# Performance work log

Measured on AMD Instinct MI355X. Metric: run time of the kernel, lower is better.

The kernel has to match this reference:

```python
import jax, jax.numpy as jnp
import numpy as np

N = 50000

def _add_self_loops(edge_index, n):
    loop = jnp.arange(n, dtype=edge_index.dtype)
    src = jnp.concatenate([edge_index[0], loop])
    dst = jnp.concatenate([edge_index[1], loop])
    return src, dst

def _gcn_layer(x, src, dst, norm, W, b, n):
    h = x @ W                                  # [N, out]
    msg = h[src] * norm[:, None]               # [E+N, out] gather + scale
    out = jax.ops.segment_sum(msg, dst, num_segments=n)  # scatter-add
    return out + b

def _gcn_norm(src, dst, n):
    # symmetric normalization D^-1/2 (A+I) D^-1/2 (PyG GCNConv default)
    deg = jax.ops.segment_sum(jnp.ones_like(dst, dtype=jnp.float32), dst, num_segments=n)
    dinv = jnp.where(deg > 0, jax.lax.rsqrt(jnp.maximum(deg, 1.0)), 0.0)
    return dinv[src] * dinv[dst]

def setup_inputs() -> dict:
    key = jax.random.key(0)
    ks = jax.random.split(key, 4)
    x = jax.random.normal(ks[0], (N, 64), dtype=jnp.float32)
    edge_index = jax.random.randint(ks[1], (2, 800000), 0, N, dtype=jnp.int64)
    W1 = jax.random.normal(ks[2], (64, 128), dtype=jnp.float32) * (1.0 / np.sqrt(64))
    b1 = jnp.zeros((128,), dtype=jnp.float32)
    W2 = jax.random.normal(ks[3], (128, 64), dtype=jnp.float32) * (1.0 / np.sqrt(128))
    b2 = jnp.zeros((64,), dtype=jnp.float32)
    return {"x": x, "edge_index": edge_index, "W1": W1, "b1": b1, "W2": W2, "b2": b2}

def reference(x, edge_index, W1, b1, W2, b2):
    n = x.shape[0]
    src, dst = _add_self_loops(edge_index, n)
    norm = _gcn_norm(src, dst, n)
    h = _gcn_layer(x, src, dst, norm, W1, b1, n)
    h = jax.nn.relu(h)
    # dropout with p=0 (eval) is identity
    h = _gcn_layer(h, src, dst, norm, W2, b2, n)
    return jax.nn.relu(h)
```

## Files before the change

### kernel.cpp

```cpp
#include <hip/hip_runtime.h>
#include <hip/hip_fp16.h>
#include <cstddef>
#include <cstdint>

static inline int divup(int a, int b) { return (a + b - 1) / b; }

#define CAP 64
#define EPB 4096
#define BSH 8

typedef _Float16 h2v __attribute__((ext_vector_type(2)));

__device__ inline float fdot2f(unsigned int a, unsigned int b, float c) {
#if __has_builtin(__builtin_amdgcn_fdot2)
    return __builtin_amdgcn_fdot2(__builtin_bit_cast(h2v, a),
                                  __builtin_bit_cast(h2v, b), c, false);
#else
    __half2 ha = __builtin_bit_cast(__half2, a);
    __half2 hb = __builtin_bit_cast(__half2, b);
    float2 fa = __half22float2(ha), fb = __half22float2(hb);
    return fmaf(fa.y, fb.y, fmaf(fa.x, fb.x, c));
#endif
}

__global__ __launch_bounds__(256) void k_bin(const int* __restrict__ src,
                                             const int* __restrict__ dst,
                                             int2* __restrict__ staging,
                                             int* __restrict__ runoff,
                                             int* __restrict__ runlen,
                                             int E, int nbuck, int NB) {
    __shared__ int hist[256];
    __shared__ int scan[256];
    const int t = threadIdx.x;
    const int blk = blockIdx.x;
    const int e0 = blk * EPB;

    int2 ed[16];
    int cb[16];
    #pragma unroll
    for (int j = 0; j < 16; ++j) {
        int idx = e0 + j * 256 + t;
        if (idx < E) {
            ed[j].x = src[idx];
            ed[j].y = dst[idx];
            cb[j] = ed[j].y >> BSH;
        } else {
            cb[j] = -1;
        }
    }
    hist[t] = 0;
    __syncthreads();
    #pragma unroll
    for (int j = 0; j < 16; ++j)
        if (cb[j] >= 0) atomicAdd(&hist[cb[j]], 1);
    __syncthreads();
    scan[t] = hist[t];
    __syncthreads();
    for (int d = 1; d < 256; d <<= 1) {
        int v = (t >= d) ? scan[t - d] : 0;
        __syncthreads();
        scan[t] += v;
        __syncthreads();
    }
    int base = scan[t] - hist[t];
    if (t < nbuck) {
        runoff[t * NB + blk] = base;
        runlen[t * NB + blk] = hist[t];
    }
    hist[t] = base;
    __syncthreads();
    #pragma unroll
    for (int j = 0; j < 16; ++j) {
        if (cb[j] >= 0) {
            int p = atomicAdd(&hist[cb[j]], 1);
            staging[e0 + p] = ed[j];
        }
    }
}

__global__ __launch_bounds__(256) void k_build(const int2* __restrict__ staging,
                                               const int* __restrict__ runoff,
                                               const int* __restrict__ runlen,
                                               const float* __restrict__ x,
                                               int* __restrict__ eidx,
                                               int* __restrict__ cnt,
                                               float* __restrict__ dinv,
                                               __half* __restrict__ xh,
                                               int n, int NB) {
    __shared__ int runstart[512 + 1];
    __shared__ int runbase[512];
    __shared__ int cnt_l[256];
    __shared__ float sdinv[256];
    const int t = threadIdx.x;
    const int b = blockIdx.x;
    const int node0 = b << BSH;

    for (int r = t; r < NB; r += 256) {
        runbase[r] = runoff[b * NB + r];
        runstart[r] = runlen[b * NB + r];
    }
    cnt_l[t] = 0;
    __syncthreads();
    if (t == 0) {
        int run = 0;
        for (int r = 0; r < NB; ++r) { int l = runstart[r]; runstart[r] = run; run += l; }
        runstart[NB] = run;
    }
    __syncthreads();
    const int L = runstart[NB];
    for (int i = t; i < L; i += 256) {
        int lo = 0, hi = NB - 1;
        while (lo < hi) { int mid = (lo + hi + 1) >> 1; if (runstart[mid] <= i) lo = mid; else hi = mid - 1; }
        int2 ed = staging[lo * EPB + runbase[lo] + (i - runstart[lo])];
        int p = atomicAdd(&cnt_l[ed.y - node0], 1);
        if (p < CAP) eidx[(size_t)ed.y * CAP + p] = ed.x;
    }
    __syncthreads();
    int node = node0 + t;
    float di_t = rsqrtf((float)(cnt_l[t] + 1));
    sdinv[t] = di_t;
    if (node < n) {
        cnt[node] = cnt_l[t];
        dinv[node] = di_t;
    }
    __syncthreads();
    for (int i = t; i < 256 * 16; i += 256) {
        int lr = i >> 4, c4 = (i & 15) * 4;
        int nd = node0 + lr;
        if (nd < n) {
            float4 v = *reinterpret_cast<const float4*>(x + (size_t)nd * 64 + c4);
            float di = sdinv[lr];
            __half2 h0 = __floats2half2_rn(v.x * di, v.y * di);
            __half2 h1 = __floats2half2_rn(v.z * di, v.w * di);
            *reinterpret_cast<__half2*>(xh + (size_t)nd * 64 + c4)     = h0;
            *reinterpret_cast<__half2*>(xh + (size_t)nd * 64 + c4 + 2) = h1;
        }
    }
}

__device__ inline void acc8(uint4 u, float a[8]) {
    float2 f0 = __half22float2(*reinterpret_cast<const __half2*>(&u.x));
    float2 f1 = __half22float2(*reinterpret_cast<const __half2*>(&u.y));
    float2 f2 = __half22float2(*reinterpret_cast<const __half2*>(&u.z));
    float2 f3 = __half22float2(*reinterpret_cast<const __half2*>(&u.w));
    a[0] += f0.x; a[1] += f0.y; a[2] += f1.x; a[3] += f1.y;
    a[4] += f2.x; a[5] += f2.y; a[6] += f3.x; a[7] += f3.y;
}

template <bool FINAL>
__global__ __launch_bounds__(256) void k_aggh(const int* __restrict__ cnt,
                                              const int* __restrict__ eidx,
                                              const __half* __restrict__ in16,
                                              const float* __restrict__ dinv,
                                              const float* __restrict__ bias,
                                              void* __restrict__ outp, int n) {
    int t = blockIdx.x * blockDim.x + threadIdx.x;
    int node = t >> 3;
    if (node >= n) return;
    int lane = t & 7;
    const int hoff = lane * 8;
    float a[8] = {0.f, 0.f, 0.f, 0.f, 0.f, 0.f, 0.f, 0.f};
    acc8(*reinterpret_cast<const uint4*>(in16 + (size_t)node * 64 + hoff), a);
    const int b = node * CAP;
    const int eN = b + min(cnt[node], CAP);
    int e = b;
    for (; e + 4 <= eN; e += 4) {
        int s0 = __builtin_nontemporal_load(eidx + e);
        int s1 = __builtin_nontemporal_load(eidx + e + 1);
        int s2 = __builtin_nontemporal_load(eidx + e + 2);
        int s3 = __builtin_nontemporal_load(eidx + e + 3);
        uint4 u0 = *reinterpret_cast<const uint4*>(in16 + (size_t)s0 * 64 + hoff);
        uint4 u1 = *reinterpret_cast<const uint4*>(in16 + (size_t)s1 * 64 + hoff);
        uint4 u2 = *reinterpret_cast<const uint4*>(in16 + (size_t)s2 * 64 + hoff);
        uint4 u3 = *reinterpret_cast<const uint4*>(in16 + (size_t)s3 * 64 + hoff);
        acc8(u0, a); acc8(u1, a); acc8(u2, a); acc8(u3, a);
    }
    for (; e < eN; ++e) {
        int s = __builtin_nontemporal_load(eidx + e);
        acc8(*reinterpret_cast<const uint4*>(in16 + (size_t)s * 64 + hoff), a);
    }
    float di = dinv[node];
    if (FINAL) {
        float* out64 = (float*)outp;
        float4 r0, r1;
        const float4 b0 = *reinterpret_cast<const float4*>(bias + hoff);
        const float4 b1 = *reinterpret_cast<const float4*>(bias + hoff + 4);
        r0.x = fmaxf(fmaf(a[0], di, b0.x), 0.f); r0.y = fmaxf(fmaf(a[1], di, b0.y), 0.f);
        r0.z = fmaxf(fmaf(a[2], di, b0.z), 0.f); r0.w = fmaxf(fmaf(a[3], di, b0.w), 0.f);
        r1.x = fmaxf(fmaf(a[4], di, b1.x), 0.f); r1.y = fmaxf(fmaf(a[5], di, b1.y), 0.f);
        r1.z = fmaxf(fmaf(a[6], di, b1.z), 0.f); r1.w = fmaxf(fmaf(a[7], di, b1.w), 0.f);
        *reinterpret_cast<float4*>(out64 + (size_t)node * 64 + hoff)     = r0;
        *reinterpret_cast<float4*>(out64 + (size_t)node * 64 + hoff + 4) = r1;
    } else {
        unsigned int* out16 = (unsigned int*)outp;
        __half2 p0 = __floats2half2_rn(a[0] * di, a[1] * di);
        __half2 p1 = __floats2half2_rn(a[2] * di, a[3] * di);
        __half2 p2 = __floats2half2_rn(a[4] * di, a[5] * di);
        __half2 p3 = __floats2half2_rn(a[6] * di, a[7] * di);
        uint4 o;
        o.x = __builtin_bit_cast(unsigned int, p0);
        o.y = __builtin_bit_cast(unsigned int, p1);
        o.z = __builtin_bit_cast(unsigned int, p2);
        o.w = __builtin_bit_cast(unsigned int, p3);
        *reinterpret_cast<uint4*>(out16 + (size_t)node * 32 + lane * 4) = o;
    }
}

__global__ void k_wconv(const float* __restrict__ W1, const float* __restrict__ W2,
                        unsigned int* __restrict__ w1p, unsigned int* __restrict__ w2p) {
    int i = blockIdx.x * blockDim.x + threadIdx.x;
    if (i < 32 * 128) {
        int kp = i >> 7, c = i & 127;
        __half2 h = __floats2half2_rn(W1[(size_t)(2 * kp) * 128 + c], W1[(size_t)(2 * kp + 1) * 128 + c]);
        w1p[i] = __builtin_bit_cast(unsigned int, h);
    } else if (i < 32 * 128 + 64 * 64) {
        int j = i - 32 * 128;
        int kp = j >> 6, c = j & 63;
        __half2 h = __floats2half2_rn(W2[(size_t)(2 * kp) * 64 + c], W2[(size_t)(2 * kp + 1) * 64 + c]);
        w2p[j] = __builtin_bit_cast(unsigned int, h);
    }
}

__global__ __launch_bounds__(256) void k_mlp(const __half* __restrict__ axh,
                                             const unsigned int* __restrict__ w1p,
                                             const unsigned int* __restrict__ w2p,
                                             const float* __restrict__ b1,
                                             const float* __restrict__ dinv,
                                             __half* __restrict__ hs2h, int n) {
    __shared__ unsigned int sW1[32 * 128];
    __shared__ unsigned int sW2[64 * 64];
    __shared__ unsigned int sA[32 * 68];
    __shared__ unsigned int sH[64 * 68];
    const int t = threadIdx.x;
    const int r0 = blockIdx.x * 64;
    {
        uint4* d1 = reinterpret_cast<uint4*>(sW1);
        const uint4* s1 = reinterpret_cast<const uint4*>(w1p);
        for (int i = t; i < 1024; i += 256) d1[i] = s1[i];
        uint4* d2 = reinterpret_cast<uint4*>(sW2);
        const uint4* s2 = reinterpret_cast<const uint4*>(w2p);
        for (int i = t; i < 1024; i += 256) d2[i] = s2[i];
    }
    const unsigned int* axu = reinterpret_cast<const unsigned int*>(axh);
    for (int i = t; i < 2048; i += 256) {
        int row = i >> 5, kp = i & 31;
        int gr = r0 + row;
        sA[kp * 68 + row] = (gr < n) ? axu[(size_t)gr * 32 + kp] : 0u;
    }
    __syncthreads();
    const int tx = t & 15, ty = t >> 4;
    float acc[4][8] = {};
    #pragma unroll 8
    for (int kp = 0; kp < 32; ++kp) {
        uint4 a4 = *reinterpret_cast<const uint4*>(&sA[kp * 68 + ty * 4]);
        uint4 wA = *reinterpret_cast<const uint4*>(&sW1[kp * 128 + tx * 4]);
        uint4 wB = *reinterpret_cast<const uint4*>(&sW1[kp * 128 + 64 + tx * 4]);
        unsigned int av[4] = {a4.x, a4.y, a4.z, a4.w};
        unsigned int wv[8] = {wA.x, wA.y, wA.z, wA.w, wB.x, wB.y, wB.z, wB.w};
        #pragma unroll
        for (int r = 0; r < 4; ++r)
            #pragma unroll
            for (int c = 0; c < 8; ++c)
                acc[r][c] = fdot2f(av[r], wv[c], acc[r][c]);
    }
    const float4 bb0 = *reinterpret_cast<const float4*>(b1 + tx * 4);
    const float4 bb1 = *reinterpret_cast<const float4*>(b1 + 64 + tx * 4);
    #pragma unroll
    for (int r = 0; r < 4; ++r) {
        int row = ty * 4 + r;
        float h0 = fmaxf(acc[r][0] + bb0.x, 0.f), h1 = fmaxf(acc[r][1] + bb0.y, 0.f);
        float h2 = fmaxf(acc[r][2] + bb0.z, 0.f), h3 = fmaxf(acc[r][3] + bb0.w, 0.f);
        float h4 = fmaxf(acc[r][4] + bb1.x, 0.f), h5 = fmaxf(acc[r][5] + bb1.y, 0.f);
        float h6 = fmaxf(acc[r][6] + bb1.z, 0.f), h7 = fmaxf(acc[r][7] + bb1.w, 0.f);
        __half2 p;
        p = __floats2half2_rn(h0, h1); sH[(2 * tx + 0) * 68 + row]  = __builtin_bit_cast(unsigned int, p);
        p = __floats2half2_rn(h2, h3); sH[(2 * tx + 1) * 68 + row]  = __builtin_bit_cast(unsigned int, p);
        p = __floats2half2_rn(h4, h5); sH[(32 + 2 * tx) * 68 + row] = __builtin_bit_cast(unsigned int, p);
        p = __floats2half2_rn(h6, h7); sH[(33 + 2 * tx) * 68 + row] = __builtin_bit_cast(unsigned int, p);
    }
    __syncthreads();
    float acc2[4][4] = {};
    #pragma unroll 8
    for (int kp = 0; kp < 64; ++kp) {
        uint4 a4 = *reinterpret_cast<const uint4*>(&sH[kp * 68 + ty * 4]);
        uint4 w4 = *reinterpret_cast<const uint4*>(&sW2[kp * 64 + tx * 4]);
        unsigned int av[4] = {a4.x, a4.y, a4.z, a4.w};
        unsigned int wv[4] = {w4.x, w4.y, w4.z, w4.w};
        #pragma unroll
        for (int r = 0; r < 4; ++r)
            #pragma unroll
            for (int c = 0; c < 4; ++c)
                acc2[r][c] = fdot2f(av[r], wv[c], acc2[r][c]);
    }
    #pragma unroll
    for (int r = 0; r < 4; ++r) {
        int row = r0 + ty * 4 + r;
        if (row < n) {
            float di = dinv[row];
            __half2 q0 = __floats2half2_rn(acc2[r][0] * di, acc2[r][1] * di);
            __half2 q1 = __floats2half2_rn(acc2[r][2] * di, acc2[r][3] * di);
            uint2 o;
            o.x = __builtin_bit_cast(unsigned int, q0);
            o.y = __builtin_bit_cast(unsigned int, q1);
            *reinterpret_cast<uint2*>(hs2h + (size_t)row * 64 + tx * 4) = o;
        }
    }
}

extern "C" void kernel_launch(void* const* d_in, const int* in_sizes, int n_in,
                              void* d_out, int out_size, void* d_ws, size_t ws_size,
                              hipStream_t stream) {
    const float* x  = (const float*)d_in[0];
    const int*   ei = (const int*)d_in[1];
    const float* W1 = (const float*)d_in[2];
    const float* b1 = (const float*)d_in[3];
    const float* W2 = (const float*)d_in[4];
    const float* b2 = (const float*)d_in[5];
    float* out = (float*)d_out;

    const int n = in_sizes[0] / 64;
    const int E = in_sizes[1] / 2;
    const int* src = ei;
    const int* dst = ei + E;

    const int NB = divup(E, EPB);
    const int nbuck = divup(n, 1 << BSH);

    char* ws = (char*)d_ws;
    size_t off = 0;
    auto alloc = [&](size_t bytes) { void* p = ws + off; off = (off + bytes + 255) & ~(size_t)255; return p; };
    int*    cnt     = (int*)   alloc((size_t)n * 4);
    float*  dinv    = (float*) alloc((size_t)n * 4);
    int2*   staging = (int2*)  alloc((size_t)NB * EPB * 8);
    int*    runoff  = (int*)   alloc((size_t)nbuck * NB * 4);
    int*    runlen  = (int*)   alloc((size_t)nbuck * NB * 4);
    int*    eidx    = (int*)   alloc((size_t)n * CAP * 4);
    __half* xh      = (__half*)alloc((size_t)n * 64 * 2);
    __half* axh     = (__half*)alloc((size_t)n * 64 * 2);
    unsigned int* w1p = (unsigned int*)alloc(32 * 128 * 4);
    unsigned int* w2p = (unsigned int*)alloc(64 * 64 * 4);
    __half* hs2h    = xh;

    k_bin  <<<NB, 256, 0, stream>>>(src, dst, staging, runoff, runlen, E, nbuck, NB);
    k_build<<<nbuck, 256, 0, stream>>>(staging, runoff, runlen, x, eidx, cnt, dinv, xh, n, NB);
    k_wconv<<<32, 256, 0, stream>>>(W1, W2, w1p, w2p);

    k_aggh<false><<<divup(n * 8, 256), 256, 0, stream>>>(cnt, eidx, xh, dinv, nullptr, axh, n);

    k_mlp<<<divup(n, 64), 256, 0, stream>>>(axh, w1p, w2p, b1, dinv, hs2h, n);

    k_aggh<true><<<divup(n * 8, 256), 256, 0, stream>>>(cnt, eidx, hs2h, dinv, b2, out, n);
}
```

Before: 117.2 us.

## Fuse first aggregation into MLP, fold weight conversion into binning, parallel scan

```diff
diff --git a/kernel.cpp b/kernel.cpp
--- a/kernel.cpp
+++ b/kernel.cpp
@@ -28,11 +28,32 @@
                                              int2* __restrict__ staging,
                                              int* __restrict__ runoff,
                                              int* __restrict__ runlen,
+                                             const float* __restrict__ W1,
+                                             const float* __restrict__ W2,
+                                             unsigned int* __restrict__ w1p,
+                                             unsigned int* __restrict__ w2p,
                                              int E, int nbuck, int NB) {
+    const int t = threadIdx.x;
+    const int blk = blockIdx.x;
+    if (blk == NB) {
+        for (int i = t; i < 32 * 128 + 64 * 64; i += 256) {
+            if (i < 32 * 128) {
+                int kp = i >> 7, c = i & 127;
+                __half2 h = __floats2half2_rn(W1[(size_t)(2 * kp) * 128 + c],
+                                              W1[(size_t)(2 * kp + 1) * 128 + c]);
+                w1p[i] = __builtin_bit_cast(unsigned int, h);
+            } else {
+                int j = i - 32 * 128;
+                int kp = j >> 6, c = j & 63;
+                __half2 h = __floats2half2_rn(W2[(size_t)(2 * kp) * 64 + c],
+                                              W2[(size_t)(2 * kp + 1) * 64 + c]);
+                w2p[j] = __builtin_bit_cast(unsigned int, h);
+            }
+        }
+        return;
+    }
     __shared__ int hist[256];
     __shared__ int scan[256];
-    const int t = threadIdx.x;
-    const int blk = blockIdx.x;
     const int e0 = blk * EPB;
 
     int2 ed[16];
@@ -89,23 +110,26 @@
                                                int n, int NB) {
     __shared__ int runstart[512 + 1];
     __shared__ int runbase[512];
+    __shared__ int sscan[256];
     __shared__ int cnt_l[256];
     __shared__ float sdinv[256];
     const int t = threadIdx.x;
     const int b = blockIdx.x;
     const int node0 = b << BSH;
 
-    for (int r = t; r < NB; r += 256) {
-        runbase[r] = runoff[b * NB + r];
-        runstart[r] = runlen[b * NB + r];
-    }
+    for (int r = t; r < NB; r += 256) runbase[r] = runoff[b * NB + r];
+    int myv = (t < NB) ? runlen[b * NB + t] : 0;
+    sscan[t] = myv;
     cnt_l[t] = 0;
     __syncthreads();
-    if (t == 0) {
-        int run = 0;
-        for (int r = 0; r < NB; ++r) { int l = runstart[r]; runstart[r] = run; run += l; }
-        runstart[NB] = run;
-    }
+    for (int d = 1; d < 256; d <<= 1) {
+        int u = (t >= d) ? sscan[t - d] : 0;
+        __syncthreads();
+        sscan[t] += u;
+        __syncthreads();
+    }
+    if (t < NB) runstart[t] = sscan[t] - myv;
+    if (t == 255) runstart[NB] = sscan[255];
     __syncthreads();
     const int L = runstart[NB];
     for (int i = t; i < L; i += 256) {
@@ -147,13 +171,12 @@
     a[4] += f2.x; a[5] += f2.y; a[6] += f3.x; a[7] += f3.y;
 }
 
-template <bool FINAL>
-__global__ __launch_bounds__(256) void k_aggh(const int* __restrict__ cnt,
+__global__ __launch_bounds__(256) void k_agg2(const int* __restrict__ cnt,
                                               const int* __restrict__ eidx,
                                               const __half* __restrict__ in16,
                                               const float* __restrict__ dinv,
                                               const float* __restrict__ bias,
-                                              void* __restrict__ outp, int n) {
+                                              float* __restrict__ out64, int n) {
     int t = blockIdx.x * blockDim.x + threadIdx.x;
     int node = t >> 3;
     if (node >= n) return;
@@ -180,48 +203,20 @@
         acc8(*reinterpret_cast<const uint4*>(in16 + (size_t)s * 64 + hoff), a);
     }
     float di = dinv[node];
-    if (FINAL) {
-        float* out64 = (float*)outp;
-        float4 r0, r1;
-        const float4 b0 = *reinterpret_cast<const float4*>(bias + hoff);
-        const float4 b1 = *reinterpret_cast<const float4*>(bias + hoff + 4);
-        r0.x = fmaxf(fmaf(a[0], di, b0.x), 0.f); r0.y = fmaxf(fmaf(a[1], di, b0.y), 0.f);
-        r0.z = fmaxf(fmaf(a[2], di, b0.z), 0.f); r0.w = fmaxf(fmaf(a[3], di, b0.w), 0.f);
-        r1.x = fmaxf(fmaf(a[4], di, b1.x), 0.f); r1.y = fmaxf(fmaf(a[5], di, b1.y), 0.f);
-        r1.z = fmaxf(fmaf(a[6], di, b1.z), 0.f); r1.w = fmaxf(fmaf(a[7], di, b1.w), 0.f);
-        *reinterpret_cast<float4*>(out64 + (size_t)node * 64 + hoff)     = r0;
-        *reinterpret_cast<float4*>(out64 + (size_t)node * 64 + hoff + 4) = r1;
-    } else {
-        unsigned int* out16 = (unsigned int*)outp;
-        __half2 p0 = __floats2half2_rn(a[0] * di, a[1] * di);
-        __half2 p1 = __floats2half2_rn(a[2] * di, a[3] * di);
-        __half2 p2 = __floats2half2_rn(a[4] * di, a[5] * di);
-        __half2 p3 = __floats2half2_rn(a[6] * di, a[7] * di);
-        uint4 o;
-        o.x = __builtin_bit_cast(unsigned int, p0);
-        o.y = __builtin_bit_cast(unsigned int, p1);
-        o.z = __builtin_bit_cast(unsigned int, p2);
-        o.w = __builtin_bit_cast(unsigned int, p3);
-        *reinterpret_cast<uint4*>(out16 + (size_t)node * 32 + lane * 4) = o;
-    }
-}
-
-__global__ void k_wconv(const float* __restrict__ W1, const float* __restrict__ W2,
-                        unsigned int* __restrict__ w1p, unsigned int* __restrict__ w2p) {
-    int i = blockIdx.x * blockDim.x + threadIdx.x;
-    if (i < 32 * 128) {
-        int kp = i >> 7, c = i & 127;
-        __half2 h = __floats2half2_rn(W1[(size_t)(2 * kp) * 128 + c], W1[(size_t)(2 * kp + 1) * 128 + c]);
-        w1p[i] = __builtin_bit_cast(unsigned int, h);
-    } else if (i < 32 * 128 + 64 * 64) {
-        int j = i - 32 * 128;
-        int kp = j >> 6, c = j & 63;
-        __half2 h = __floats2half2_rn(W2[(size_t)(2 * kp) * 64 + c], W2[(size_t)(2 * kp + 1) * 64 + c]);
-        w2p[j] = __builtin_bit_cast(unsigned int, h);
-    }
-}
-
-__global__ __launch_bounds__(256) void k_mlp(const __half* __restrict__ axh,
+    float4 r0, r1;
+    const float4 b0 = *reinterpret_cast<const float4*>(bias + hoff);
+    const float4 b1 = *reinterpret_cast<const float4*>(bias + hoff + 4);
+    r0.x = fmaxf(fmaf(a[0], di, b0.x), 0.f); r0.y = fmaxf(fmaf(a[1], di, b0.y), 0.f);
+    r0.z = fmaxf(fmaf(a[2], di, b0.z), 0.f); r0.w = fmaxf(fmaf(a[3], di, b0.w), 0.f);
+    r1.x = fmaxf(fmaf(a[4], di, b1.x), 0.f); r1.y = fmaxf(fmaf(a[5], di, b1.y), 0.f);
+    r1.z = fmaxf(fmaf(a[6], di, b1.z), 0.f); r1.w = fmaxf(fmaf(a[7], di, b1.w), 0.f);
+    *reinterpret_cast<float4*>(out64 + (size_t)node * 64 + hoff)     = r0;
+    *reinterpret_cast<float4*>(out64 + (size_t)node * 64 + hoff + 4) = r1;
+}
+
+__global__ __launch_bounds__(256) void k_mlp(const __half* __restrict__ xh,
+                                             const int* __restrict__ cnt,
+                                             const int* __restrict__ eidx,
                                              const unsigned int* __restrict__ w1p,
                                              const unsigned int* __restrict__ w2p,
                                              const float* __restrict__ b1,
@@ -241,11 +236,46 @@
         const uint4* s2 = reinterpret_cast<const uint4*>(w2p);
         for (int i = t; i < 1024; i += 256) d2[i] = s2[i];
     }
-    const unsigned int* axu = reinterpret_cast<const unsigned int*>(axh);
-    for (int i = t; i < 2048; i += 256) {
-        int row = i >> 5, kp = i & 31;
-        int gr = r0 + row;
-        sA[kp * 68 + row] = (gr < n) ? axu[(size_t)gr * 32 + kp] : 0u;
+    #pragma unroll
+    for (int h = 0; h < 2; ++h) {
+        int task = h * 256 + t;
+        int row = task >> 3;
+        int lane = task & 7;
+        int node = r0 + row;
+        float a[8] = {0.f, 0.f, 0.f, 0.f, 0.f, 0.f, 0.f, 0.f};
+        float di = 0.f;
+        if (node < n) {
+            const int hoff = lane * 8;
+            acc8(*reinterpret_cast<const uint4*>(xh + (size_t)node * 64 + hoff), a);
+            const int b = node * CAP;
+            const int eN = b + min(cnt[node], CAP);
+            int e = b;
+            for (; e + 4 <= eN; e += 4) {
+                int s0 = __builtin_nontemporal_load(eidx + e);
+                int s1 = __builtin_nontemporal_load(eidx + e + 1);
+                int s2 = __builtin_nontemporal_load(eidx + e + 2);
+                int s3 = __builtin_nontemporal_load(eidx + e + 3);
+                uint4 u0 = *reinterpret_cast<const uint4*>(xh + (size_t)s0 * 64 + hoff);
+                uint4 u1 = *reinterpret_cast<const uint4*>(xh + (size_t)s1 * 64 + hoff);
+                uint4 u2 = *reinterpret_cast<const uint4*>(xh + (size_t)s2 * 64 + hoff);
+                uint4 u3 = *reinterpret_cast<const uint4*>(xh + (size_t)s3 * 64 + hoff);
+                acc8(u0, a); acc8(u1, a); acc8(u2, a); acc8(u3, a);
+            }
+            for (; e < eN; ++e) {
+                int s = __builtin_nontemporal_load(eidx + e);
+                acc8(*reinterpret_cast<const uint4*>(xh + (size_t)s * 64 + hoff), a);
+            }
+            di = dinv[node];
+        }
+        int kpb = lane * 4;
+        __half2 p0 = __floats2half2_rn(a[0] * di, a[1] * di);
+        __half2 p1 = __floats2half2_rn(a[2] * di, a[3] * di);
+        __half2 p2 = __floats2half2_rn(a[4] * di, a[5] * di);
+        __half2 p3 = __floats2half2_rn(a[6] * di, a[7] * di);
+        sA[(kpb + 0) * 68 + row] = __builtin_bit_cast(unsigned int, p0);
+        sA[(kpb + 1) * 68 + row] = __builtin_bit_cast(unsigned int, p1);
+        sA[(kpb + 2) * 68 + row] = __builtin_bit_cast(unsigned int, p2);
+        sA[(kpb + 3) * 68 + row] = __builtin_bit_cast(unsigned int, p3);
     }
     __syncthreads();
     const int tx = t & 15, ty = t >> 4;
@@ -336,18 +366,14 @@
     int*    runlen  = (int*)   alloc((size_t)nbuck * NB * 4);
     int*    eidx    = (int*)   alloc((size_t)n * CAP * 4);
     __half* xh      = (__half*)alloc((size_t)n * 64 * 2);
-    __half* axh     = (__half*)alloc((size_t)n * 64 * 2);
+    __half* hs2h    = (__half*)alloc((size_t)n * 64 * 2);
     unsigned int* w1p = (unsigned int*)alloc(32 * 128 * 4);
     unsigned int* w2p = (unsigned int*)alloc(64 * 64 * 4);
-    __half* hs2h    = xh;
-
-    k_bin  <<<NB, 256, 0, stream>>>(src, dst, staging, runoff, runlen, E, nbuck, NB);
+
+    k_bin  <<<NB + 1, 256, 0, stream>>>(src, dst, staging, runoff, runlen, W1, W2, w1p, w2p, E, nbuck, NB);
     k_build<<<nbuck, 256, 0, stream>>>(staging, runoff, runlen, x, eidx, cnt, dinv, xh, n, NB);
-    k_wconv<<<32, 256, 0, stream>>>(W1, W2, w1p, w2p);
-
-    k_aggh<false><<<divup(n * 8, 256), 256, 0, stream>>>(cnt, eidx, xh, dinv, nullptr, axh, n);
-
-    k_mlp<<<divup(n, 64), 256, 0, stream>>>(axh, w1p, w2p, b1, dinv, hs2h, n);
-
-    k_aggh<true><<<divup(n * 8, 256), 256, 0, stream>>>(cnt, eidx, hs2h, dinv, b2, out, n);
-}
+
+    k_mlp<<<divup(n, 64), 256, 0, stream>>>(xh, cnt, eidx, w1p, w2p, b1, dinv, hs2h, n);
+
+    k_agg2<<<divup(n * 8, 256), 256, 0, stream>>>(cnt, eidx, hs2h, dinv, b2, out, n);
+}
```

Result: slower. 119.6 us (+2.1%).
